# Optimization experiments

Hardware: AMD Instinct MI355X
Metric: run time of the kernel (lower is better)

## Reference

```python
import jax, jax.numpy as jnp
import numpy as np

D_MODEL = 1024
NUM_HEADS = 16
D_HEAD = D_MODEL // NUM_HEADS
ROPE_THETA = 10000.0


def _rope(x, pos):
    # x: [..., S, d_head]; rotate consecutive pairs (2i, 2i+1)
    half = x.shape[-1] // 2
    inv_freq = ROPE_THETA ** (-jnp.arange(half, dtype=jnp.float32) * 2.0 / x.shape[-1])
    ang = pos[:, None].astype(jnp.float32) * inv_freq[None, :]  # [S, half]
    cos, sin = jnp.cos(ang), jnp.sin(ang)
    x1, x2 = x[..., 0::2], x[..., 1::2]
    r1 = x1 * cos - x2 * sin
    r2 = x1 * sin + x2 * cos
    return jnp.stack([r1, r2], axis=-1).reshape(x.shape)


def setup_inputs() -> dict:
    key = jax.random.key(0)
    ks = jax.random.split(key, 5)
    s = 1.0 / np.sqrt(D_MODEL)
    return {
        "q_weight": jax.random.normal(ks[0], (D_MODEL, D_MODEL), jnp.float32) * s,
        "k_weight": jax.random.normal(ks[1], (D_MODEL, D_MODEL), jnp.float32) * s,
        "v_weight": jax.random.normal(ks[2], (D_MODEL, D_MODEL), jnp.float32) * s,
        "o_weight": jax.random.normal(ks[3], (D_MODEL, D_MODEL), jnp.float32) * s,
        "in_features": jax.random.normal(ks[4], (2, 2048, D_MODEL), jnp.float32),
    }


def reference(q_weight, k_weight, v_weight, o_weight, in_features):
    S = in_features.shape[-2]
    qw = q_weight.reshape(NUM_HEADS, D_HEAD, D_MODEL)
    kw = k_weight.reshape(NUM_HEADS, D_HEAD, D_MODEL)
    vw = v_weight.reshape(NUM_HEADS, D_HEAD, D_MODEL)
    # [B, H, S, d_head]
    q = jnp.einsum('bsj,nhj->bnsh', in_features, qw)
    k = jnp.einsum('bsj,nhj->bnsh', in_features, kw)
    v = jnp.einsum('bsj,nhj->bnsh', in_features, vw)
    pos = jnp.arange(S)
    q = _rope(q, pos)
    k = _rope(k, pos)
    scale = 1.0 / jnp.sqrt(jnp.asarray(D_HEAD, dtype=q.dtype))
    scores = jnp.einsum('bnqh,bnkh->bnqk', q, k) * scale  # [B,H,S,S]
    causal = jnp.tril(jnp.ones((S, S), dtype=bool))
    scores = jnp.where(causal, scores, jnp.asarray(-jnp.inf, dtype=scores.dtype))
    attn = jax.nn.softmax(scores, axis=-1)
    out = jnp.einsum('bnqk,bnkh->bnqh', attn, v)  # [B,H,S,d_head]
    out = jnp.swapaxes(out, -2, -3).reshape(*out.shape[:-3], S, D_MODEL)
    return jnp.einsum('ji,bki->bkj', o_weight, out)
```

## Files before the change

### kernel.cpp

```cpp
#include <hip/hip_runtime.h>
#include <math.h>

typedef __attribute__((ext_vector_type(8))) short bf16x8;
typedef __attribute__((ext_vector_type(4))) short bf16x4;
typedef __attribute__((ext_vector_type(4))) float f32x4;
typedef __attribute__((ext_vector_type(2))) unsigned int u32x2;

static constexpr int D_MODEL = 1024;
static constexpr int SEQ = 2048;
static constexpr int BATCH = 2;
static constexpr int M_TOT = BATCH * SEQ;

__device__ __forceinline__ unsigned short f2bf(float f) {
  unsigned int u = __builtin_bit_cast(unsigned int, f);
  u += 0x7fffu + ((u >> 16) & 1u);
  return (unsigned short)(u >> 16);
}

__device__ __forceinline__ unsigned int cvtpk(float lo, float hi) {
  unsigned int r;
  asm volatile("v_cvt_pk_bf16_f32 %0, %1, %2" : "=v"(r) : "v"(lo), "v"(hi));
  return r;
}

__device__ __forceinline__ void gld16(const unsigned short* g, unsigned short* l) {
  __builtin_amdgcn_global_load_lds(
      (const __attribute__((address_space(1))) unsigned int*)g,
      (__attribute__((address_space(3))) unsigned int*)l, 16, 0, 0);
}

__global__ void cvt_f32_bf16(const float* __restrict__ src,
                             unsigned short* __restrict__ dst, int n4) {
  int i = blockIdx.x * blockDim.x + threadIdx.x;
  if (i >= n4) return;
  const float4 v = reinterpret_cast<const float4*>(src)[i];
  ushort4 o;
  o.x = f2bf(v.x); o.y = f2bf(v.y); o.z = f2bf(v.z); o.w = f2bf(v.w);
  reinterpret_cast<ushort4*>(dst)[i] = o;
}

__global__ void cvt_weights(const float* __restrict__ qw, const float* __restrict__ kw,
                            const float* __restrict__ vw, const float* __restrict__ ow,
                            unsigned short* __restrict__ dst) {
  int i = blockIdx.x * blockDim.x + threadIdx.x;
  const int which = i >> 18;
  const int off = i & 262143;
  const float* src = (which == 0) ? qw : (which == 1) ? kw : (which == 2) ? vw : ow;
  const float4 v = reinterpret_cast<const float4*>(src)[off];
  ushort4 o;
  o.x = f2bf(v.x); o.y = f2bf(v.y); o.z = f2bf(v.z); o.w = f2bf(v.w);
  reinterpret_cast<ushort4*>(dst)[i] = o;
}

__global__ void rope_tables(float2* __restrict__ ct2) {
  int idx = blockIdx.x * blockDim.x + threadIdx.x;
  int s = idx >> 5;
  int p = idx & 31;
  float inv_freq = powf(10000.0f, -(float)p / 32.0f);
  float ang = (float)s * inv_freq;
  int psw = p ^ (((s >> 2) & 1) << 3);
  float2 cs; cs.x = cosf(ang); cs.y = sinf(ang);
  ct2[s * 32 + psw] = cs;
}

template <int BM, int BN, int MODE>
__global__ __launch_bounds__(256, 2)
void gemm2(const unsigned short* __restrict__ A,
           const unsigned short* __restrict__ W,
           unsigned short* __restrict__ Qd,
           unsigned short* __restrict__ Kd,
           unsigned short* __restrict__ Vd,
           float* __restrict__ Fd,
           const float2* __restrict__ ct2) {
  constexpr int MI = BM / 32, NI = BN / 32;
  constexpr int NKT = D_MODEL / 64;
  constexpr int LOADS = BM / 32 + BN / 32;
  __shared__ __align__(16) unsigned short smem[2 * (BM + BN) * 64];
  unsigned short* Asm = smem;
  unsigned short* Bsm = smem + 2 * BM * 64;
  const int tid  = threadIdx.x;
  const int lane = tid & 63;
  const int wave = tid >> 6;
  const int wm = wave >> 1, wn = wave & 1;
  const int m0 = blockIdx.y * BM;
  const int n0 = blockIdx.x * BN;
  const int lr = lane & 15, lg = lane >> 4;

  auto stage = [&](int buf, int kt) {
    const int k0 = kt * 64;
#pragma unroll
    for (int c = 0; c < BM / 32; ++c) {
      const int ch = c * 4 + wave;
      const int row = ch * 8 + (lane >> 3);
      gld16(&A[(size_t)(m0 + row) * D_MODEL + k0 + ((lane & 7) ^ (row & 7)) * 8],
            &Asm[buf * BM * 64 + ch * 512]);
    }
#pragma unroll
    for (int c = 0; c < BN / 32; ++c) {
      const int ch = c * 4 + wave;
      const int row = ch * 8 + (lane >> 3);
      gld16(&W[(size_t)(n0 + row) * D_MODEL + k0 + ((lane & 7) ^ (row & 7)) * 8],
            &Bsm[buf * BN * 64 + ch * 512]);
    }
  };

  f32x4 acc[MI][NI] = {};

  stage(0, 0);
  stage(1, 1);
  __builtin_amdgcn_sched_barrier(0);

  for (int kt = 0; kt < NKT; ++kt) {
    const int cur = kt & 1;
    if (kt + 1 < NKT) {
      if constexpr (LOADS == 8) asm volatile("s_waitcnt vmcnt(8)" ::: "memory");
      else                      asm volatile("s_waitcnt vmcnt(6)" ::: "memory");
    } else {
      asm volatile("s_waitcnt vmcnt(0)" ::: "memory");
    }
    __builtin_amdgcn_s_barrier();
    __builtin_amdgcn_sched_barrier(0);

    bf16x8 af[MI][2], bfr[NI][2];
#pragma unroll
    for (int i = 0; i < MI; ++i)
#pragma unroll
      for (int ks = 0; ks < 2; ++ks) {
        const int R = wm * (BM / 2) + i * 16 + lr;
        const int p = (ks * 4 + lg) ^ (R & 7);
        af[i][ks] = *reinterpret_cast<const bf16x8*>(&Asm[cur * BM * 64 + R * 64 + p * 8]);
      }
#pragma unroll
    for (int j = 0; j < NI; ++j)
#pragma unroll
      for (int ks = 0; ks < 2; ++ks) {
        const int R = wn * (BN / 2) + j * 16 + lr;
        const int p = (ks * 4 + lg) ^ (R & 7);
        bfr[j][ks] = *reinterpret_cast<const bf16x8*>(&Bsm[cur * BN * 64 + R * 64 + p * 8]);
      }
    asm volatile("s_waitcnt lgkmcnt(0)" ::: "memory");
    __builtin_amdgcn_sched_barrier(0);
    __builtin_amdgcn_s_barrier();
    __builtin_amdgcn_sched_barrier(0);

    if (kt + 2 < NKT) stage(cur, kt + 2);
    __builtin_amdgcn_sched_barrier(0);

#pragma unroll
    for (int ks = 0; ks < 2; ++ks)
#pragma unroll
      for (int i = 0; i < MI; ++i)
#pragma unroll
        for (int j = 0; j < NI; ++j)
          acc[i][j] = __builtin_amdgcn_mfma_f32_16x16x32_bf16(af[i][ks], bfr[j][ks], acc[i][j], 0, 0, 0);
  }

  if constexpr (MODE == 2) {
#pragma unroll
    for (int i = 0; i < MI; ++i)
#pragma unroll
      for (int j = 0; j < NI; ++j)
#pragma unroll
        for (int r = 0; r < 4; ++r) {
          const int gm = m0 + wm * (BM / 2) + i * 16 + lg * 4 + r;
          const int gc = n0 + wn * (BN / 2) + j * 16 + lr;
          Fd[(size_t)gm * D_MODEL + gc] = acc[i][j][r];
        }
  } else {
    const int t = n0 >> 10;
    const int b = m0 >> 11;
    const int s_base = m0 & 2047;
    if (t < 2) {
      unsigned short* dstQ = (t == 0) ? Qd : Kd;
      const unsigned short* gsrc = (const unsigned short*)(ct2 + (size_t)s_base * 32);
#pragma unroll
      for (int it = 0; it < 8; ++it) {
        const int ch = wave * 8 + it;
        gld16(&gsrc[ch * 512 + lane * 8], &smem[ch * 512]);
      }
      asm volatile("s_waitcnt vmcnt(0)" ::: "memory");
      __builtin_amdgcn_sched_barrier(0);
      __builtin_amdgcn_s_barrier();
      const float2* tbl = (const float2*)smem;
      const int nbase = (n0 & 1023) >> 6;
#pragma unroll
      for (int i = 0; i < MI; ++i) {
#pragma unroll
        for (int j = 0; j < NI; ++j) {
#pragma unroll
          for (int r = 0; r < 4; ++r) {
            const int sl = wm * (BM / 2) + i * 16 + lg * 4 + r;
            const int h  = j * 16 + lr;
            const int psw = (h >> 1) ^ (((sl >> 2) & 1) << 3);
            const float2 cs = tbl[sl * 32 + psw];
            float x = acc[i][j][r];
            const float part = __shfl_xor(x, 1, 64);
            x = (h & 1) ? (part * cs.y + x * cs.x) : (x * cs.x - part * cs.y);
            const int n = nbase + wn;
            dstQ[(size_t)((b * 16 + n) * SEQ + s_base + sl) * 64 + h] = f2bf(x);
          }
        }
      }
    } else {
      unsigned short* tile = smem;
      const int row = tid >> 2;
      const int ck  = tid & 3;
      for (int pass = 0; pass < 2; ++pass) {
        __builtin_amdgcn_s_barrier();
        if (wn == pass) {
#pragma unroll
          for (int i = 0; i < MI; ++i)
#pragma unroll
            for (int j = 0; j < NI; ++j)
#pragma unroll
              for (int r = 0; r < 4; ++r)
                tile[(j * 16 + lr) * 136 + wm * 64 + i * 16 + lg * 4 + r] = f2bf(acc[i][j][r]);
        }
        asm volatile("s_waitcnt lgkmcnt(0)" ::: "memory");
        __builtin_amdgcn_sched_barrier(0);
        __builtin_amdgcn_s_barrier();
        const int c = (n0 & 1023) + pass * 64 + row;
        const int n = c >> 6, h = c & 63;
        unsigned short* vrow = &Vd[(size_t)((b * 16 + n) * 64 + h) * SEQ + s_base + ck * 32];
        const unsigned short* lrow = &tile[row * 136 + ck * 32];
#pragma unroll
        for (int k = 0; k < 4; ++k)
          *reinterpret_cast<bf16x8*>(&vrow[k * 8]) = *reinterpret_cast<const bf16x8*>(&lrow[k * 8]);
      }
    }
  }
}

__global__ __launch_bounds__(256, 2)
void attn_kernel(const unsigned short* __restrict__ Q,
                 const unsigned short* __restrict__ K,
                 const unsigned short* __restrict__ Vt,
                 unsigned short* __restrict__ AO) {
  __shared__ __align__(16) unsigned short Ksh[2][4096];
  __shared__ __align__(16) unsigned short Vsh[2][4096];
  const int bn   = blockIdx.x;
  const int y    = blockIdx.y;
  const int j    = (y < 8) ? (15 - y) : (y - 8);
  const int wave = threadIdx.x >> 6;
  const int lane = threadIdx.x & 63;
  const int lr = lane & 15, lg = lane >> 4;
  const int q0 = j * 128 + wave * 32;
  const unsigned short* Qh = Q  + (size_t)bn * SEQ * 64;
  const unsigned short* Kh = K  + (size_t)bn * SEQ * 64;
  const unsigned short* Vh = Vt + (size_t)bn * 64 * SEQ;
  const int b = bn >> 4, n = bn & 15;

  const int srow8 = lane >> 3;
  const int scolb = ((lane & 7) ^ srow8) * 8;

  auto stage = [&](int buf, int k0) {
#pragma unroll
    for (int c = 0; c < 2; ++c) {
      const int ch = wave * 2 + c;
      const int row = ch * 8 + srow8;
      gld16(&Kh[(size_t)(k0 + row) * 64 + scolb], &Ksh[buf][ch * 512]);
      gld16(&Vh[(size_t)row * SEQ + k0 + scolb], &Vsh[buf][ch * 512]);
    }
  };

  constexpr float KL2E = 0.125f * 1.44269504088896f;
  const int nt = 2 * j + 2;

  bf16x8 qf[2][2];
#pragma unroll
  for (int mi = 0; mi < 2; ++mi)
#pragma unroll
    for (int ks = 0; ks < 2; ++ks)
      qf[mi][ks] = *reinterpret_cast<const bf16x8*>(
          &Qh[(size_t)(q0 + mi * 16 + lr) * 64 + ks * 32 + lg * 8]);
  asm volatile("s_waitcnt vmcnt(0)" ::: "memory");
  __builtin_amdgcn_sched_barrier(0);

  f32x4 o[2][4] = {};
  float ls[2] = {0.f, 0.f};

  stage(0, 0);
  stage(1, 64);
  __builtin_amdgcn_sched_barrier(0);

  for (int t = 0; t < nt; ++t) {
    const int cur = t & 1;
    const int k0 = t * 64;
    if (t + 1 < nt) { asm volatile("s_waitcnt vmcnt(4)" ::: "memory"); }
    else            { asm volatile("s_waitcnt vmcnt(0)" ::: "memory"); }
    __builtin_amdgcn_s_barrier();
    __builtin_amdgcn_sched_barrier(0);

    const unsigned short* Kc = &Ksh[cur][0];
    const unsigned short* Vc = &Vsh[cur][0];

    bf16x8 kf[4][2];
#pragma unroll
    for (int nj = 0; nj < 4; ++nj)
#pragma unroll
      for (int ks = 0; ks < 2; ++ks) {
        const int R = nj * 16 + lr;
        const int p = (ks * 4 + lg) ^ (R & 7);
        kf[nj][ks] = *reinterpret_cast<const bf16x8*>(&Kc[R * 64 + p * 8]);
      }
    f32x4 sf[2][4] = {};
    __builtin_amdgcn_s_setprio(1);
#pragma unroll
    for (int nj = 0; nj < 4; ++nj)
#pragma unroll
      for (int ks = 0; ks < 2; ++ks)
#pragma unroll
        for (int mi = 0; mi < 2; ++mi)
          sf[mi][nj] = __builtin_amdgcn_mfma_f32_16x16x32_bf16(kf[nj][ks], qf[mi][ks], sf[mi][nj], 0, 0, 0);
    __builtin_amdgcn_s_setprio(0);

    bf16x4 vB[4][4];
#pragma unroll
    for (int nj = 0; nj < 4; ++nj)
#pragma unroll
      for (int hf = 0; hf < 4; ++hf) {
        const int R = hf * 16 + lr;
        const int c = nj * 2 + (lg >> 1);
        const int p = ((c ^ (R & 7)) << 3) + (lg & 1) * 4;
        vB[nj][hf] = *reinterpret_cast<const bf16x4*>(&Vc[R * 64 + p]);
      }

    u32x2 w[2][4];
    if (k0 + 63 <= q0) {
#pragma unroll
      for (int mi = 0; mi < 2; ++mi)
#pragma unroll
        for (int nj = 0; nj < 4; ++nj) {
          const float p0 = __builtin_amdgcn_exp2f(sf[mi][nj][0] * KL2E);
          const float p1 = __builtin_amdgcn_exp2f(sf[mi][nj][1] * KL2E);
          const float p2 = __builtin_amdgcn_exp2f(sf[mi][nj][2] * KL2E);
          const float p3 = __builtin_amdgcn_exp2f(sf[mi][nj][3] * KL2E);
          ls[mi] += (p0 + p1) + (p2 + p3);
          w[mi][nj][0] = cvtpk(p0, p1);
          w[mi][nj][1] = cvtpk(p2, p3);
        }
    } else {
#pragma unroll
      for (int mi = 0; mi < 2; ++mi) {
        const int qrow = q0 + mi * 16 + lr;
#pragma unroll
        for (int nj = 0; nj < 4; ++nj) {
          const int kb = k0 + nj * 16 + lg * 4;
          float p[4];
#pragma unroll
          for (int r = 0; r < 4; ++r)
            p[r] = (kb + r <= qrow) ? __builtin_amdgcn_exp2f(sf[mi][nj][r] * KL2E) : 0.0f;
          ls[mi] += (p[0] + p[1]) + (p[2] + p[3]);
          w[mi][nj][0] = cvtpk(p[0], p[1]);
          w[mi][nj][1] = cvtpk(p[2], p[3]);
        }
      }
    }

    asm volatile("s_waitcnt lgkmcnt(0)" ::: "memory");
    __builtin_amdgcn_sched_barrier(0);
    __builtin_amdgcn_s_barrier();
    __builtin_amdgcn_sched_barrier(0);

    if (t + 2 < nt) stage(cur, (t + 2) * 64);
    __builtin_amdgcn_sched_barrier(0);

    __builtin_amdgcn_s_setprio(1);
#pragma unroll
    for (int nj = 0; nj < 4; ++nj)
#pragma unroll
      for (int hf = 0; hf < 4; ++hf)
#pragma unroll
        for (int mi = 0; mi < 2; ++mi)
          o[mi][hf] = __builtin_amdgcn_mfma_f32_16x16x16bf16_1k(
              __builtin_bit_cast(bf16x4, w[mi][nj]), vB[nj][hf], o[mi][hf], 0, 0, 0);
    __builtin_amdgcn_s_setprio(0);
  }

#pragma unroll
  for (int mi = 0; mi < 2; ++mi) {
    float s = ls[mi];
    s += __shfl_xor(s, 16, 64);
    s += __shfl_xor(s, 32, 64);
    ls[mi] = s;
  }
#pragma unroll
  for (int mi = 0; mi < 2; ++mi)
#pragma unroll
    for (int r = 0; r < 4; ++r) {
      const float sv = __shfl(ls[mi], lg * 4 + r, 64);
      const float inv = 1.0f / sv;
      const int srow = q0 + mi * 16 + lg * 4 + r;
#pragma unroll
      for (int hf = 0; hf < 4; ++hf) {
        const int h = hf * 16 + lr;
        AO[(size_t)(b * SEQ + srow) * D_MODEL + n * 64 + h] = f2bf(o[mi][hf][r] * inv);
      }
    }
}

extern "C" void kernel_launch(void* const* d_in, const int* in_sizes, int n_in,
                              void* d_out, int out_size, void* d_ws, size_t ws_size,
                              hipStream_t stream) {
  const float* qw = (const float*)d_in[0];
  const float* kw = (const float*)d_in[1];
  const float* vw = (const float*)d_in[2];
  const float* ow = (const float*)d_in[3];
  const float* x  = (const float*)d_in[4];

  char* ws = (char*)d_ws;
  const size_t XB = (size_t)M_TOT * D_MODEL * 2;
  const size_t WB = (size_t)D_MODEL * D_MODEL * 2;
  unsigned short* Xb  = (unsigned short*)ws;  ws += XB;
  unsigned short* Wqb = (unsigned short*)ws;  ws += WB;
  unsigned short* Wkb = (unsigned short*)ws;  ws += WB;
  unsigned short* Wvb = (unsigned short*)ws;  ws += WB;
  unsigned short* Wob = (unsigned short*)ws;  ws += WB;
  unsigned short* Qr  = (unsigned short*)ws;  ws += XB;
  unsigned short* Kr  = (unsigned short*)ws;  ws += XB;
  unsigned short* Vt  = (unsigned short*)ws;  ws += XB;
  unsigned short* AO  = (unsigned short*)ws;  ws += XB;
  float2* ct2 = (float2*)ws;  ws += (size_t)SEQ * 32 * 8;
  (void)Wkb; (void)Wvb;

  cvt_f32_bf16<<<(M_TOT * D_MODEL / 4) / 256, 256, 0, stream>>>(x, Xb, M_TOT * D_MODEL / 4);
  cvt_weights<<<(4 * D_MODEL * D_MODEL / 4) / 256, 256, 0, stream>>>(qw, kw, vw, ow, Wqb);
  rope_tables<<<(SEQ * 32) / 256, 256, 0, stream>>>(ct2);

  gemm2<128, 128, 0><<<dim3(3072 / 128, M_TOT / 128), 256, 0, stream>>>(
      Xb, Wqb, Qr, Kr, Vt, nullptr, ct2);

  attn_kernel<<<dim3(BATCH * 16, 16), 256, 0, stream>>>(Qr, Kr, Vt, AO);

  gemm2<128, 64, 2><<<dim3(D_MODEL / 64, M_TOT / 128), 256, 0, stream>>>(
      AO, Wob, nullptr, nullptr, nullptr, (float*)d_out, nullptr);
}
```

Before: 102.1 us.

## Fuse prep kernels and halve attention query tile to 64 rows

Merges the three preprocessing launches (input cast, weight cast, RoPE tables) into a single kernel to cut launch overhead. Reworks the attention kernel to use 128-thread blocks covering 64 query rows each, doubling the grid to 32 tiles per head with a reordered heavy/light tile schedule. Each wave now issues twice as many K/V staging loads, and the waitcnt is adjusted to match. Smaller blocks should improve causal load balance and occupancy, but K/V tiles are reloaded by twice as many blocks.

```diff
diff --git a/kernel.cpp b/kernel.cpp
--- a/kernel.cpp
+++ b/kernel.cpp
@@ -29,38 +29,39 @@
       (__attribute__((address_space(3))) unsigned int*)l, 16, 0, 0);
 }
 
-__global__ void cvt_f32_bf16(const float* __restrict__ src,
-                             unsigned short* __restrict__ dst, int n4) {
-  int i = blockIdx.x * blockDim.x + threadIdx.x;
-  if (i >= n4) return;
-  const float4 v = reinterpret_cast<const float4*>(src)[i];
-  ushort4 o;
-  o.x = f2bf(v.x); o.y = f2bf(v.y); o.z = f2bf(v.z); o.w = f2bf(v.w);
-  reinterpret_cast<ushort4*>(dst)[i] = o;
-}
-
-__global__ void cvt_weights(const float* __restrict__ qw, const float* __restrict__ kw,
-                            const float* __restrict__ vw, const float* __restrict__ ow,
-                            unsigned short* __restrict__ dst) {
-  int i = blockIdx.x * blockDim.x + threadIdx.x;
-  const int which = i >> 18;
-  const int off = i & 262143;
-  const float* src = (which == 0) ? qw : (which == 1) ? kw : (which == 2) ? vw : ow;
-  const float4 v = reinterpret_cast<const float4*>(src)[off];
-  ushort4 o;
-  o.x = f2bf(v.x); o.y = f2bf(v.y); o.z = f2bf(v.z); o.w = f2bf(v.w);
-  reinterpret_cast<ushort4*>(dst)[i] = o;
-}
-
-__global__ void rope_tables(float2* __restrict__ ct2) {
-  int idx = blockIdx.x * blockDim.x + threadIdx.x;
-  int s = idx >> 5;
-  int p = idx & 31;
-  float inv_freq = powf(10000.0f, -(float)p / 32.0f);
-  float ang = (float)s * inv_freq;
-  int psw = p ^ (((s >> 2) & 1) << 3);
-  float2 cs; cs.x = cosf(ang); cs.y = sinf(ang);
-  ct2[s * 32 + psw] = cs;
+__global__ void prep_all(const float* __restrict__ x,
+                         const float* __restrict__ qw, const float* __restrict__ kw,
+                         const float* __restrict__ vw, const float* __restrict__ ow,
+                         unsigned short* __restrict__ Xb,
+                         unsigned short* __restrict__ Wqb,
+                         float2* __restrict__ ct2) {
+  constexpr int NX = M_TOT * D_MODEL / 4;
+  constexpr int NW = D_MODEL * D_MODEL;
+  const int i = blockIdx.x * blockDim.x + threadIdx.x;
+  if (i < NX) {
+    const float4 v = reinterpret_cast<const float4*>(x)[i];
+    ushort4 o;
+    o.x = f2bf(v.x); o.y = f2bf(v.y); o.z = f2bf(v.z); o.w = f2bf(v.w);
+    reinterpret_cast<ushort4*>(Xb)[i] = o;
+  } else if (i < NX + NW) {
+    const int k = i - NX;
+    const int which = k >> 18;
+    const int off = k & 262143;
+    const float* src = (which == 0) ? qw : (which == 1) ? kw : (which == 2) ? vw : ow;
+    const float4 v = reinterpret_cast<const float4*>(src)[off];
+    ushort4 o;
+    o.x = f2bf(v.x); o.y = f2bf(v.y); o.z = f2bf(v.z); o.w = f2bf(v.w);
+    reinterpret_cast<ushort4*>(Wqb)[k] = o;
+  } else {
+    const int k = i - NX - NW;
+    const int s = k >> 5;
+    const int p = k & 31;
+    const float inv_freq = powf(10000.0f, -(float)p / 32.0f);
+    const float ang = (float)s * inv_freq;
+    const int psw = p ^ (((s >> 2) & 1) << 3);
+    float2 cs; cs.x = cosf(ang); cs.y = sinf(ang);
+    ct2[s * 32 + psw] = cs;
+  }
 }
 
 template <int BM, int BN, int MODE>
@@ -231,7 +232,7 @@
   }
 }
 
-__global__ __launch_bounds__(256, 2)
+__global__ __launch_bounds__(128, 2)
 void attn_kernel(const unsigned short* __restrict__ Q,
                  const unsigned short* __restrict__ K,
                  const unsigned short* __restrict__ Vt,
@@ -240,11 +241,13 @@
   __shared__ __align__(16) unsigned short Vsh[2][4096];
   const int bn   = blockIdx.x;
   const int y    = blockIdx.y;
-  const int j    = (y < 8) ? (15 - y) : (y - 8);
+  const int a    = y & 7, bsel = y >> 3;
+  const int j    = (bsel == 0) ? (31 - a) : (bsel == 1) ? (16 + a)
+                 : (bsel == 2) ? (15 - a) : a;
   const int wave = threadIdx.x >> 6;
   const int lane = threadIdx.x & 63;
   const int lr = lane & 15, lg = lane >> 4;
-  const int q0 = j * 128 + wave * 32;
+  const int q0 = j * 64 + wave * 32;
   const unsigned short* Qh = Q  + (size_t)bn * SEQ * 64;
   const unsigned short* Kh = K  + (size_t)bn * SEQ * 64;
   const unsigned short* Vh = Vt + (size_t)bn * 64 * SEQ;
@@ -255,8 +258,8 @@
 
   auto stage = [&](int buf, int k0) {
 #pragma unroll
-    for (int c = 0; c < 2; ++c) {
-      const int ch = wave * 2 + c;
+    for (int c = 0; c < 4; ++c) {
+      const int ch = wave * 4 + c;
       const int row = ch * 8 + srow8;
       gld16(&Kh[(size_t)(k0 + row) * 64 + scolb], &Ksh[buf][ch * 512]);
       gld16(&Vh[(size_t)row * SEQ + k0 + scolb], &Vsh[buf][ch * 512]);
@@ -264,7 +267,7 @@
   };
 
   constexpr float KL2E = 0.125f * 1.44269504088896f;
-  const int nt = 2 * j + 2;
+  const int nt = j + 1;
 
   bf16x8 qf[2][2];
 #pragma unroll
@@ -286,7 +289,7 @@
   for (int t = 0; t < nt; ++t) {
     const int cur = t & 1;
     const int k0 = t * 64;
-    if (t + 1 < nt) { asm volatile("s_waitcnt vmcnt(4)" ::: "memory"); }
+    if (t + 1 < nt) { asm volatile("s_waitcnt vmcnt(8)" ::: "memory"); }
     else            { asm volatile("s_waitcnt vmcnt(0)" ::: "memory"); }
     __builtin_amdgcn_s_barrier();
     __builtin_amdgcn_sched_barrier(0);
@@ -423,14 +426,13 @@
   float2* ct2 = (float2*)ws;  ws += (size_t)SEQ * 32 * 8;
   (void)Wkb; (void)Wvb;
 
-  cvt_f32_bf16<<<(M_TOT * D_MODEL / 4) / 256, 256, 0, stream>>>(x, Xb, M_TOT * D_MODEL / 4);
-  cvt_weights<<<(4 * D_MODEL * D_MODEL / 4) / 256, 256, 0, stream>>>(qw, kw, vw, ow, Wqb);
-  rope_tables<<<(SEQ * 32) / 256, 256, 0, stream>>>(ct2);
+  constexpr int PREP_ITEMS = M_TOT * D_MODEL / 4 + D_MODEL * D_MODEL + SEQ * 32;
+  prep_all<<<(PREP_ITEMS + 255) / 256, 256, 0, stream>>>(x, qw, kw, vw, ow, Xb, Wqb, ct2);
 
   gemm2<128, 128, 0><<<dim3(3072 / 128, M_TOT / 128), 256, 0, stream>>>(
       Xb, Wqb, Qr, Kr, Vt, nullptr, ct2);
 
-  attn_kernel<<<dim3(BATCH * 16, 16), 256, 0, stream>>>(Qr, Kr, Vt, AO);
+  attn_kernel<<<dim3(BATCH * 16, 32), 128, 0, stream>>>(Qr, Kr, Vt, AO);
 
   gemm2<128, 64, 2><<<dim3(D_MODEL / 64, M_TOT / 128), 256, 0, stream>>>(
       AO, Wob, nullptr, nullptr, nullptr, (float*)d_out, nullptr);
```

Result: no change. 103.8 us (+1.6%).
